# Kernel optimization log

Hardware: AMD Instinct MI355X
Metric: run time of the kernel (lower is better)

Reference implementation:

```python
import jax, jax.numpy as jnp
import numpy as np

SIZE = 64

def setup_inputs() -> dict:
    key = jax.random.key(0)
    k1, k2 = jax.random.split(key)
    x = jax.random.normal(k1, (8, 2048, SIZE * SIZE), dtype=jnp.float32)
    param = jax.random.normal(k2, (2, SIZE, SIZE, SIZE), dtype=jnp.float32)
    return {"x": x, "param": param}

def reference(x, param):
    b = param.shape[1]
    # view [..., b, b] then transpose last two dims
    xr = x.reshape(*x.shape[:-1], b, b)
    xr = jnp.swapaxes(xr, -1, -2)                       # [..., n, j]
    h = jnp.einsum('nij,...nj->...in', param[0], xr)    # [..., i, n] (acts like transpose + blockdiag matmul)
    h = jnp.einsum('nij,...nj->...in', param[1], h)     # [..., i, n]
    return h.reshape(*h.shape[:-2], b * b)
```

## Files before the change

### kernel.cpp

```cpp
#include <hip/hip_runtime.h>


typedef __bf16 bf16x8 __attribute__((ext_vector_type(8)));
typedef float f32x4 __attribute__((ext_vector_type(4)));

__device__ __forceinline__ unsigned short bf16b(float f) {
  return __builtin_bit_cast(unsigned short, (__bf16)f);
}

__global__ __launch_bounds__(256) void pack_params(const float* __restrict__ p,
                                                   __bf16* __restrict__ wp) {
  unsigned g = blockIdx.x * 256 + threadIdx.x;
  unsigned lane = g & 63;
  unsigned kb = (g >> 6) & 1;
  unsigned it = (g >> 7) & 3;
  unsigned n  = (g >> 9) & 63;
  unsigned l  = (g >> 15) & 1;
  const float* src = p + (size_t)(((l * 64 + n) * 64 + it * 16 + (lane & 15)) * 64
                                  + kb * 32 + (lane >> 4) * 8);
  f32x4 a = *(const f32x4*)(src);
  f32x4 b = *(const f32x4*)(src + 4);
  bf16x8 o;
  o[0] = (__bf16)a[0]; o[1] = (__bf16)a[1]; o[2] = (__bf16)a[2]; o[3] = (__bf16)a[3];
  o[4] = (__bf16)b[0]; o[5] = (__bf16)b[1]; o[6] = (__bf16)b[2]; o[7] = (__bf16)b[3];
  *(bf16x8*)(wp + (size_t)g * 8) = o;
}

__device__ __forceinline__ bf16x8 load_bfrag(const __bf16* __restrict__ wp,
                                             const float* __restrict__ param,
                                             int use_packed,
                                             unsigned l, unsigned n, unsigned it,
                                             unsigned kb, unsigned lane) {
  if (use_packed) {
    size_t idx = ((size_t)((((l * 64 + n) * 4 + it) * 2 + kb) * 64 + lane)) * 8;
    return *(const bf16x8*)(wp + idx);
  } else {
    unsigned mr = lane & 15, quad = lane >> 4;
    const float* s = param + (size_t)(((l * 64 + n) * 64 + it * 16 + mr) * 64
                                      + kb * 32 + quad * 8);
    f32x4 q0 = *(const f32x4*)s;
    f32x4 q1 = *(const f32x4*)(s + 4);
    bf16x8 o;
    o[0] = (__bf16)q0[0]; o[1] = (__bf16)q0[1]; o[2] = (__bf16)q0[2]; o[3] = (__bf16)q0[3];
    o[4] = (__bf16)q1[0]; o[5] = (__bf16)q1[1]; o[6] = (__bf16)q1[2]; o[7] = (__bf16)q1[3];
    return o;
  }
}

__global__ __launch_bounds__(512, 4) void monarch_kernel(const float* __restrict__ x,
                                                         const float* __restrict__ param,
                                                         const __bf16* __restrict__ wp,
                                                         int use_packed,
                                                         float* __restrict__ out) {
  __shared__ __align__(16) unsigned char smem[81920];
  const unsigned YS = 65536u;

  unsigned tid = threadIdx.x;
  unsigned wave = tid >> 6, lane = tid & 63;
  unsigned mr = lane & 15, quad = lane >> 4;
  unsigned rA = mr & 7;
  unsigned r0 = blockIdx.x * 8;

#pragma unroll 2
  for (int itr = 0; itr < 8; ++itr) {
    unsigned p = itr * 512 + tid;
    unsigned r = p >> 9;
    unsigned rem = p & 511;
    unsigned jp = rem >> 4;
    unsigned n4r = rem & 15;
    unsigned j0 = jp * 2;
    const f32x4* base = (const f32x4*)(x + (size_t)(r0 + r) * 4096);
    f32x4 a = base[j0 * 16 + n4r];
    f32x4 b = base[(j0 + 1) * 16 + n4r];
#pragma unroll
    for (int d = 0; d < 4; ++d) {
      unsigned n = n4r * 4 + d;
      unsigned up = (j0 >> 3) ^ r ^ ((n >> 3) & 7);
      unsigned byte = n * 1024 + r * 128 + up * 16 + (j0 & 7) * 2;
      unsigned v = (unsigned)bf16b(a[d]) | ((unsigned)bf16b(b[d]) << 16);
      *(unsigned*)(smem + byte) = v;
    }
  }
  __syncthreads();

  for (int i1t = 0; i1t < 4; ++i1t) {
    unsigned n1b = wave * 8;
    bf16x8 nb0 = load_bfrag(wp, param, use_packed, 0, n1b, i1t, 0, lane);
    bf16x8 nb1 = load_bfrag(wp, param, use_packed, 0, n1b, i1t, 1, lane);
#pragma unroll 2
    for (int t = 0; t < 8; ++t) {
      unsigned n1 = n1b + t;
      bf16x8 b0 = nb0, b1 = nb1;
      if (t < 7) {
        nb0 = load_bfrag(wp, param, use_packed, 0, n1 + 1, i1t, 0, lane);
        nb1 = load_bfrag(wp, param, use_packed, 0, n1 + 1, i1t, 1, lane);
      }
      unsigned c8 = (n1 >> 3) & 7;
      bf16x8 a0 = *(const bf16x8*)(smem + n1 * 1024 + rA * 128 + ((quad ^ rA ^ c8) * 16));
      bf16x8 a1 = *(const bf16x8*)(smem + n1 * 1024 + rA * 128 + (((4 + quad) ^ rA ^ c8) * 16));
      f32x4 acc = {0.f, 0.f, 0.f, 0.f};
      acc = __builtin_amdgcn_mfma_f32_16x16x32_bf16(a0, b0, acc, 0, 0, 0);
      acc = __builtin_amdgcn_mfma_f32_16x16x32_bf16(a1, b1, acc, 0, 0, 0);
      if (quad < 2) {
        unsigned i1r = mr;
#pragma unroll
        for (int rg = 0; rg < 4; ++rg) {
          unsigned r = quad * 4 + rg;
          unsigned upy = (n1 >> 3) ^ r ^ (i1r & 7);
          unsigned byte = YS + i1r * 1024 + r * 128 + upy * 16 + (n1 & 7) * 2;
          *(unsigned short*)(smem + byte) = bf16b(acc[rg]);
        }
      }
    }
    __syncthreads();

    unsigned n2rp = wave * 2;
    bf16x8 A2[2][2];
#pragma unroll
    for (int q2 = 0; q2 < 2; ++q2) {
      unsigned i1r = n2rp + q2;
#pragma unroll
      for (int kb = 0; kb < 2; ++kb) {
        unsigned u = kb * 4 + quad;
        unsigned upy = u ^ rA ^ (i1r & 7);
        A2[q2][kb] = *(const bf16x8*)(smem + YS + i1r * 1024 + rA * 128 + upy * 16);
      }
    }
    __syncthreads();

    float* outs = (float*)(smem + YS);
#pragma unroll
    for (int h = 0; h < 2; ++h) {
#pragma unroll
      for (int q2 = 0; q2 < 2; ++q2) {
        unsigned n2r = n2rp + q2;
        unsigned n2 = i1t * 16 + n2r;
#pragma unroll
        for (int i2th = 0; i2th < 2; ++i2th) {
          unsigned i2t = h * 2 + i2th;
          bf16x8 b0 = load_bfrag(wp, param, use_packed, 1, n2, i2t, 0, lane);
          bf16x8 b1 = load_bfrag(wp, param, use_packed, 1, n2, i2t, 1, lane);
          f32x4 acc = {0.f, 0.f, 0.f, 0.f};
          acc = __builtin_amdgcn_mfma_f32_16x16x32_bf16(A2[q2][0], b0, acc, 0, 0, 0);
          acc = __builtin_amdgcn_mfma_f32_16x16x32_bf16(A2[q2][1], b1, acc, 0, 0, 0);
          if (quad < 2) {
            unsigned i2 = i2t * 16 + mr;
            unsigned i2h = i2 - h * 32;
            unsigned n2s = n2r ^ (i2 & 15);
#pragma unroll
            for (int rg = 0; rg < 4; ++rg) {
              unsigned r = quad * 4 + rg;
              outs[r * 512 + i2h * 16 + n2s] = acc[rg];
            }
          }
        }
      }
      __syncthreads();
      for (int k = 0; k < 8; ++k) {
        unsigned L = k * 512 + tid;
        unsigned r = L >> 9;
        unsigned rem = L & 511;
        unsigned i2h = rem >> 4;
        unsigned n2sp = rem & 15;
        unsigned i2 = h * 32 + i2h;
        unsigned n2 = i1t * 16 + (n2sp ^ (i2 & 15));
        out[(size_t)(r0 + r) * 4096 + i2 * 64 + n2] = outs[L];
      }
      __syncthreads();
    }
  }
}

extern "C" void kernel_launch(void* const* d_in, const int* in_sizes, int n_in,
                              void* d_out, int out_size, void* d_ws, size_t ws_size,
                              hipStream_t stream) {
  const float* x = (const float*)d_in[0];
  const float* param = (const float*)d_in[1];
  float* out = (float*)d_out;

  const size_t PACK_BYTES = (size_t)2 * 64 * 64 * 64 * 2;
  int use_packed = (d_ws != nullptr && ws_size >= PACK_BYTES) ? 1 : 0;
  __bf16* wp = (__bf16*)d_ws;

  if (use_packed) {
    pack_params<<<256, 256, 0, stream>>>(param, wp);
  }
  int rows = in_sizes[0] / 4096;
  int grid = rows / 8;
  monarch_kernel<<<grid, 512, 0, stream>>>(x, param, wp, use_packed, out);
}
```

Baseline: 525.5 us.

## Cache first-stage A fragments in registers and vectorize output stores

Loads all first-stage x fragments from LDS into registers once, before the i1t loop. This frees the x LDS region to serve as a full-width output staging buffer. The second stage now computes all 64 output columns per tile in one pass instead of two halves, which removes several barriers. The output is written with 16-byte vector global stores after an in-register unswizzle, replacing scalar 4-byte stores. The cost is higher register pressure (64 extra VGPRs for the cached fragments), which under the 512-thread launch bound may reduce occupancy or cause spills.

Measured after the change: 927.3 us. +76.4%, slower.

```diff
diff --git a/kernel.cpp b/kernel.cpp
--- a/kernel.cpp
+++ b/kernel.cpp
@@ -83,11 +83,23 @@
   }
   __syncthreads();
 
+  bf16x8 A1[8][2];
+#pragma unroll
+  for (int t = 0; t < 8; ++t) {
+    unsigned n1 = wave * 8 + t;
+    unsigned c8 = (n1 >> 3) & 7;
+    const unsigned char* xb = smem + n1 * 1024 + rA * 128;
+    A1[t][0] = *(const bf16x8*)(xb + ((quad ^ rA ^ c8) * 16));
+    A1[t][1] = *(const bf16x8*)(xb + (((4 + quad) ^ rA ^ c8) * 16));
+  }
+  float* outs = (float*)smem;
+  unsigned n2rp = wave * 2;
+
   for (int i1t = 0; i1t < 4; ++i1t) {
     unsigned n1b = wave * 8;
     bf16x8 nb0 = load_bfrag(wp, param, use_packed, 0, n1b, i1t, 0, lane);
     bf16x8 nb1 = load_bfrag(wp, param, use_packed, 0, n1b, i1t, 1, lane);
-#pragma unroll 2
+#pragma unroll
     for (int t = 0; t < 8; ++t) {
       unsigned n1 = n1b + t;
       bf16x8 b0 = nb0, b1 = nb1;
@@ -95,12 +107,9 @@
         nb0 = load_bfrag(wp, param, use_packed, 0, n1 + 1, i1t, 0, lane);
         nb1 = load_bfrag(wp, param, use_packed, 0, n1 + 1, i1t, 1, lane);
       }
-      unsigned c8 = (n1 >> 3) & 7;
-      bf16x8 a0 = *(const bf16x8*)(smem + n1 * 1024 + rA * 128 + ((quad ^ rA ^ c8) * 16));
-      bf16x8 a1 = *(const bf16x8*)(smem + n1 * 1024 + rA * 128 + (((4 + quad) ^ rA ^ c8) * 16));
       f32x4 acc = {0.f, 0.f, 0.f, 0.f};
-      acc = __builtin_amdgcn_mfma_f32_16x16x32_bf16(a0, b0, acc, 0, 0, 0);
-      acc = __builtin_amdgcn_mfma_f32_16x16x32_bf16(a1, b1, acc, 0, 0, 0);
+      acc = __builtin_amdgcn_mfma_f32_16x16x32_bf16(A1[t][0], b0, acc, 0, 0, 0);
+      acc = __builtin_amdgcn_mfma_f32_16x16x32_bf16(A1[t][1], b1, acc, 0, 0, 0);
       if (quad < 2) {
         unsigned i1r = mr;
 #pragma unroll
@@ -114,7 +123,6 @@
     }
     __syncthreads();
 
-    unsigned n2rp = wave * 2;
     bf16x8 A2[2][2];
 #pragma unroll
     for (int q2 = 0; q2 < 2; ++q2) {
@@ -126,47 +134,51 @@
         A2[q2][kb] = *(const bf16x8*)(smem + YS + i1r * 1024 + rA * 128 + upy * 16);
       }
     }
-    __syncthreads();
-
-    float* outs = (float*)(smem + YS);
-#pragma unroll
-    for (int h = 0; h < 2; ++h) {
-#pragma unroll
-      for (int q2 = 0; q2 < 2; ++q2) {
-        unsigned n2r = n2rp + q2;
-        unsigned n2 = i1t * 16 + n2r;
-#pragma unroll
-        for (int i2th = 0; i2th < 2; ++i2th) {
-          unsigned i2t = h * 2 + i2th;
-          bf16x8 b0 = load_bfrag(wp, param, use_packed, 1, n2, i2t, 0, lane);
-          bf16x8 b1 = load_bfrag(wp, param, use_packed, 1, n2, i2t, 1, lane);
-          f32x4 acc = {0.f, 0.f, 0.f, 0.f};
-          acc = __builtin_amdgcn_mfma_f32_16x16x32_bf16(A2[q2][0], b0, acc, 0, 0, 0);
-          acc = __builtin_amdgcn_mfma_f32_16x16x32_bf16(A2[q2][1], b1, acc, 0, 0, 0);
-          if (quad < 2) {
-            unsigned i2 = i2t * 16 + mr;
-            unsigned i2h = i2 - h * 32;
-            unsigned n2s = n2r ^ (i2 & 15);
-#pragma unroll
-            for (int rg = 0; rg < 4; ++rg) {
-              unsigned r = quad * 4 + rg;
-              outs[r * 512 + i2h * 16 + n2s] = acc[rg];
-            }
+#pragma unroll
+    for (int q2 = 0; q2 < 2; ++q2) {
+      unsigned n2r = n2rp + q2;
+      unsigned n2 = i1t * 16 + n2r;
+#pragma unroll
+      for (int i2t = 0; i2t < 4; ++i2t) {
+        bf16x8 b0 = load_bfrag(wp, param, use_packed, 1, n2, i2t, 0, lane);
+        bf16x8 b1 = load_bfrag(wp, param, use_packed, 1, n2, i2t, 1, lane);
+        f32x4 acc = {0.f, 0.f, 0.f, 0.f};
+        acc = __builtin_amdgcn_mfma_f32_16x16x32_bf16(A2[q2][0], b0, acc, 0, 0, 0);
+        acc = __builtin_amdgcn_mfma_f32_16x16x32_bf16(A2[q2][1], b1, acc, 0, 0, 0);
+        if (quad < 2) {
+          unsigned i2 = i2t * 16 + mr;
+          unsigned n2s = n2r ^ mr;
+#pragma unroll
+          for (int rg = 0; rg < 4; ++rg) {
+            unsigned r = quad * 4 + rg;
+            outs[r * 1024 + i2 * 16 + n2s] = acc[rg];
           }
         }
       }
-      __syncthreads();
-      for (int k = 0; k < 8; ++k) {
-        unsigned L = k * 512 + tid;
-        unsigned r = L >> 9;
-        unsigned rem = L & 511;
-        unsigned i2h = rem >> 4;
-        unsigned n2sp = rem & 15;
-        unsigned i2 = h * 32 + i2h;
-        unsigned n2 = i1t * 16 + (n2sp ^ (i2 & 15));
-        out[(size_t)(r0 + r) * 4096 + i2 * 64 + n2] = outs[L];
-      }
-      __syncthreads();
+    }
+    __syncthreads();
+
+#pragma unroll
+    for (int it2 = 0; it2 < 4; ++it2) {
+      unsigned q = it2 * 512 + tid;
+      unsigned r = q >> 8;
+      unsigned rem = q & 255;
+      unsigned i2 = rem >> 2;
+      unsigned g = (rem & 3) * 4;
+      f32x4 v = *(const f32x4*)(outs + r * 1024 + i2 * 16 + g);
+      unsigned c = i2 & 3;
+      bool s1 = (c & 1) != 0, s2 = (c & 2) != 0;
+      float a0 = s1 ? v[1] : v[0];
+      float a1 = s1 ? v[0] : v[1];
+      float a2 = s1 ? v[3] : v[2];
+      float a3 = s1 ? v[2] : v[3];
+      f32x4 w;
+      w[0] = s2 ? a2 : a0;
+      w[1] = s2 ? a3 : a1;
+      w[2] = s2 ? a0 : a2;
+      w[3] = s2 ? a1 : a3;
+      unsigned n2g = i1t * 16 + ((g ^ (i2 & 15)) & 12u);
+      *(f32x4*)(out + (size_t)(r0 + r) * 4096 + i2 * 64 + n2g) = w;
     }
   }
 }
```
